# Optimization experiments

Hardware: AMD Instinct MI355X
Metric: run time of the kernel (lower is better)

Reference implementation:

```python
import math
import jax, jax.numpy as jnp
import numpy as np

B, N, TOKEN_DIM = 8, 8192, 512
NODE_DIM = 64
MAX_NODES = 64
SCORE_HIDDEN = 64


def setup_inputs() -> dict:
    key = jax.random.key(0)
    ks = jax.random.split(key, 8)
    s = lambda k, shape, fan_in: jax.random.normal(k, shape, jnp.float32) / np.sqrt(fan_in)
    return {
        "token_feats": jax.random.normal(ks[0], (B, N, TOKEN_DIM), jnp.float32),
        "score_w1": s(ks[1], (TOKEN_DIM, SCORE_HIDDEN), TOKEN_DIM),
        "score_b1": jnp.zeros((SCORE_HIDDEN,), jnp.float32),
        "score_w2": s(ks[2], (SCORE_HIDDEN, 1), SCORE_HIDDEN),
        "score_b2": jnp.zeros((1,), jnp.float32),
        "t2n_w": s(ks[3], (TOKEN_DIM, NODE_DIM), TOKEN_DIM),
        "n2t_w": s(ks[4], (NODE_DIM, TOKEN_DIM), NODE_DIM),
        "gcn_w1": s(ks[5], (NODE_DIM, NODE_DIM), NODE_DIM),
        "gcn_w2": s(ks[6], (NODE_DIM, NODE_DIM), NODE_DIM),
    }


def reference(token_feats, score_w1, score_b1, score_w2, score_b2,
              t2n_w, n2t_w, gcn_w1, gcn_w2):
    Bn, Nn, d = token_feats.shape
    M = MAX_NODES
    eps = 1e-6

    # --- node selection (scores -> threshold -> top-k among selected) ---
    h = jax.nn.relu(jnp.einsum('bnd,dh->bnh', token_feats, score_w1) + score_b1)
    scores = (jnp.einsum('bnh,ho->bno', h, score_w2) + score_b2)[..., 0]  # [B,N]
    mean = scores.mean(axis=1, keepdims=True)
    std = scores.std(axis=1, keepdims=True)  # unbiased=False (population)
    thr = mean + 0.5 * std
    count = jnp.sum(scores > thr, axis=1)  # [B]
    fallback_k = min(M, max(4, Nn // 16))
    take_k = jnp.where(count == 0, fallback_k, jnp.minimum(count, M))  # [B]

    _, top_idx = jax.lax.top_k(scores, M)  # [B,M] highest scores; set == torch's selection
    node_mask = jnp.arange(M)[None, :] < take_k[:, None]  # [B,M] bool
    maskf = node_mask.astype(token_feats.dtype)

    gathered = jnp.take_along_axis(token_feats, top_idx[..., None], axis=1)  # [B,M,d]
    H0 = jnp.einsum('bmd,dk->bmk', gathered, t2n_w) * maskf[..., None]  # [B,M,node_dim]

    # --- cosine-similarity adjacency, masked, self-loops, row-normalized ---
    nrm = jnp.maximum(jnp.linalg.norm(H0, axis=-1, keepdims=True), eps)
    Hn = H0 / nrm
    A = jax.nn.relu(jnp.einsum('bik,bjk->bij', Hn, Hn))
    A = A * (maskf[:, :, None] * maskf[:, None, :])
    A = A + jnp.eye(M, dtype=A.dtype)[None] * maskf[:, None, :]
    A = A / jnp.maximum(A.sum(axis=-1, keepdims=True), 1e-6)

    # --- two-layer GCN (no bias) ---
    x = jax.nn.relu(jnp.einsum('bij,bjk,kl->bil', A, H0, gcn_w1))
    Hg = jax.nn.relu(jnp.einsum('bij,bjk,kl->bil', A, x, gcn_w2))  # [B,M,node_dim]

    # --- attention scatter-back to tokens ---
    token_proj = jnp.einsum('bnd,dk->bnk', token_feats, t2n_w)  # [B,N,node_dim]
    logits = jnp.einsum('bnk,bmk->bnm', token_proj, Hg) / math.sqrt(NODE_DIM)
    attn = jax.nn.softmax(logits, axis=-1)
    injected = jnp.einsum('bnm,bmk->bnk', attn, Hg)
    back = jnp.einsum('bnk,kd->bnd', injected, n2t_w)
    return token_feats + back
```

## Files before the change

### kernel.cpp

```cpp
#include <hip/hip_runtime.h>
#include <hip/hip_bf16.h>

#define B_ 8
#define N_ 8192
#define D_ 512
#define M_ 64

typedef unsigned short u16;
typedef unsigned int u32;
typedef __attribute__((ext_vector_type(8))) short bf16x8;
typedef __attribute__((ext_vector_type(4))) float f32x4;

__device__ __forceinline__ u16 f2bf(float f) {
  u32 u = __float_as_uint(f);
  u += 0x7FFFu + ((u >> 16) & 1u);
  return (u16)(u >> 16);
}
__device__ __forceinline__ float bf2f(u16 h) {
  return __uint_as_float(((u32)h) << 16);
}

__device__ __forceinline__ int bfrag_idx(int kd, int c, int ncols16) {
  int sub = (kd >> 5) * ncols16 + (c >> 4);
  int lane = (c & 15) + 16 * ((kd & 15) >> 2);
  int e = (kd & 3) + 4 * ((kd >> 4) & 1);
  return sub * 512 + lane * 8 + e;
}

__device__ __forceinline__ int kslot(int ln, int e) {
  return (e & 3) + 4 * (ln >> 4) + 16 * (e >> 2);
}

__device__ __forceinline__ bf16x8 pack8(float4 v0, float4 v1) {
  bf16x8 a;
  a[0] = (short)f2bf(v0.x); a[1] = (short)f2bf(v0.y);
  a[2] = (short)f2bf(v0.z); a[3] = (short)f2bf(v0.w);
  a[4] = (short)f2bf(v1.x); a[5] = (short)f2bf(v1.y);
  a[6] = (short)f2bf(v1.z); a[7] = (short)f2bf(v1.w);
  return a;
}

__global__ __launch_bounds__(256) void k_prep(
    const float* __restrict__ t2n, const float* __restrict__ n2t,
    const float* __restrict__ W1, const float* __restrict__ g1,
    const float* __restrict__ g2,
    u16* __restrict__ t2nf, u16* __restrict__ n2tf,
    u16* __restrict__ W1h, u16* __restrict__ W1l,
    u16* __restrict__ g1f, u16* __restrict__ g2f)
{
  const int gid = blockIdx.x * 256 + threadIdx.x;
  const int stride = gridDim.x * 256;
  for (int s = gid; s < 512 * 64; s += stride) {
    const int k = s >> 6, c = s & 63;
    const int idx = bfrag_idx(k, c, 4);
    t2nf[idx] = f2bf(t2n[s]);
    const float w = W1[s];
    const u16 wh = f2bf(w);
    W1h[idx] = wh;
    W1l[idx] = f2bf(w - bf2f(wh));
  }
  for (int s = gid; s < 64 * 512; s += stride) {
    const int k = s >> 9, c = s & 511;
    n2tf[bfrag_idx(k, c, 32)] = f2bf(n2t[s]);
  }
  for (int s = gid; s < 4096; s += stride) {
    const int k = s >> 6, c = s & 63;
    g1f[bfrag_idx(k, c, 4)] = f2bf(g1[s]);
    g2f[bfrag_idx(k, c, 4)] = f2bf(g2[s]);
  }
}

__global__ __launch_bounds__(256, 4) void k_sp(
    const float* __restrict__ X, const u16* __restrict__ W1h,
    const u16* __restrict__ W1l, const u16* __restrict__ t2nf,
    const float* __restrict__ b1, const float* __restrict__ w2,
    const float* __restrict__ b2, float* __restrict__ scores,
    float* __restrict__ outStash)
{
  __shared__ __align__(16) u16 sB[2][6144];
  __shared__ __align__(16) u16 sAf[4096];
  const int tid = threadIdx.x;
  const int t0 = blockIdx.x * 64;
  const int wv = tid >> 6, ln = tid & 63;
  const int lq = ln >> 4, lr = ln & 15;
  u16* mySf = &sAf[wv * 1024];
  const float* xr = X + (size_t)(t0 + 16 * wv + lr) * D_;

  f32x4 acc[4], accP[4];
  #pragma unroll
  for (int cb = 0; cb < 4; ++cb) {
    acc[cb] = (f32x4){0.f, 0.f, 0.f, 0.f};
    accP[cb] = (f32x4){0.f, 0.f, 0.f, 0.f};
  }

  auto gsrc = [&](int f, int kb) -> const u16* {
    const int cb = f / 3, mat = f % 3;
    const u16* mp = (mat == 0) ? W1h : (mat == 1) ? W1l : t2nf;
    return mp + (kb * 4 + cb) * 512 + ln * 8;
  };

  bf16x8 wr[3];
  #pragma unroll
  for (int j = 0; j < 3; ++j)
    *(bf16x8*)&sB[0][(j * 4 + wv) * 512 + ln * 8] = *(const bf16x8*)gsrc(j * 4 + wv, 0);
  #pragma unroll
  for (int j = 0; j < 3; ++j) wr[j] = *(const bf16x8*)gsrc(j * 4 + wv, 1);
  float4 va0 = *(const float4*)(xr + 4 * lq);
  float4 va1 = *(const float4*)(xr + 16 + 4 * lq);
  __syncthreads();

  for (int kb = 0; kb < 16; ++kb) {
    const int cur = kb & 1;
    if (kb < 15) {
      #pragma unroll
      for (int j = 0; j < 3; ++j)
        *(bf16x8*)&sB[cur ^ 1][(j * 4 + wv) * 512 + ln * 8] = wr[j];
    }
    if (kb < 14) {
      #pragma unroll
      for (int j = 0; j < 3; ++j) wr[j] = *(const bf16x8*)gsrc(j * 4 + wv, kb + 2);
    }
    const float4 v0 = va0, v1 = va1;
    if (kb < 15) {
      va0 = *(const float4*)(xr + 32 * (kb + 1) + 4 * lq);
      va1 = *(const float4*)(xr + 32 * (kb + 1) + 16 + 4 * lq);
    }
    const float xs[8] = {v0.x, v0.y, v0.z, v0.w, v1.x, v1.y, v1.z, v1.w};
    bf16x8 ah, al;
    #pragma unroll
    for (int e = 0; e < 8; ++e) {
      const u16 h = f2bf(xs[e]);
      ah[e] = (short)h;
      al[e] = (short)f2bf(xs[e] - bf2f(h));
    }
    #pragma unroll
    for (int cb = 0; cb < 4; ++cb) {
      const bf16x8 bh = *(const bf16x8*)&sB[cur][(cb * 3 + 0) * 512 + ln * 8];
      const bf16x8 bl = *(const bf16x8*)&sB[cur][(cb * 3 + 1) * 512 + ln * 8];
      const bf16x8 bt = *(const bf16x8*)&sB[cur][(cb * 3 + 2) * 512 + ln * 8];
      acc[cb]  = __builtin_amdgcn_mfma_f32_16x16x32_bf16(ah, bh, acc[cb], 0, 0, 0);
      acc[cb]  = __builtin_amdgcn_mfma_f32_16x16x32_bf16(ah, bl, acc[cb], 0, 0, 0);
      acc[cb]  = __builtin_amdgcn_mfma_f32_16x16x32_bf16(al, bh, acc[cb], 0, 0, 0);
      accP[cb] = __builtin_amdgcn_mfma_f32_16x16x32_bf16(ah, bt, accP[cb], 0, 0, 0);
    }
    __syncthreads();
  }

  float b1v[4], w2v[4];
  #pragma unroll
  for (int cb = 0; cb < 4; ++cb) {
    const int col = cb * 16 + lr;
    b1v[cb] = b1[col]; w2v[cb] = w2[col];
  }
  const float b2v = b2[0];
  #pragma unroll
  for (int r = 0; r < 4; ++r) {
    float p = 0.f;
    #pragma unroll
    for (int cb = 0; cb < 4; ++cb) {
      const float h = fmaxf(acc[cb][r] + b1v[cb], 0.f);
      p = fmaf(h, w2v[cb], p);
    }
    p += __shfl_xor(p, 1); p += __shfl_xor(p, 2);
    p += __shfl_xor(p, 4); p += __shfl_xor(p, 8);
    if (lr == 0) scores[t0 + wv * 16 + 4 * lq + r] = p + b2v;
  }

  #pragma unroll
  for (int cb = 0; cb < 4; ++cb)
    #pragma unroll
    for (int r = 0; r < 4; ++r) {
      const int idx = (cb >> 1) * 512 + (4 * lq + r + 16 * (lr >> 2)) * 8 +
                      (lr & 3) + 4 * (cb & 1);
      mySf[idx] = f2bf(accP[cb][r]);
    }
  u16* stash = (u16*)(outStash + (size_t)blockIdx.x * 32768);
  #pragma unroll
  for (int kb2 = 0; kb2 < 2; ++kb2)
    *(bf16x8*)&stash[wv * 1024 + kb2 * 512 + ln * 8] =
        *(const bf16x8*)&mySf[kb2 * 512 + ln * 8];
}

__global__ __launch_bounds__(1024) void k_select(
    const float* __restrict__ scores, int* __restrict__ top_idx,
    int* __restrict__ take_k)
{
  __shared__ u32 hist[2048];
  __shared__ float redf[34];
  __shared__ u32 redu[16];
  __shared__ u32 scanp[16];
  __shared__ int sPivotBin;
  __shared__ u32 sTake, sNA, sCntA, sCntT;
  __shared__ int candIdx[64];
  __shared__ u32 candKey[64];
  __shared__ int tieIdx[1024];
  __shared__ u32 tieKey[1024];
  const int b = blockIdx.x, tid = threadIdx.x;
  const int wv = tid >> 6, ln = tid & 63;
  const float* s = scores + (size_t)b * N_;

  hist[tid] = 0; hist[tid + 1024] = 0;
  if (tid == 0) { sCntA = 0; sCntT = 0; }

  float v[8]; u32 key[8];
  float sum = 0.f, sq = 0.f;
  #pragma unroll
  for (int j = 0; j < 8; ++j) {
    v[j] = s[tid + j * 1024];
    sum += v[j]; sq = fmaf(v[j], v[j], sq);
    const u32 u = __float_as_uint(v[j]);
    key[j] = u ^ ((u32)((int)u >> 31) | 0x80000000u);
  }
  #pragma unroll
  for (int off = 32; off > 0; off >>= 1) {
    sum += __shfl_xor(sum, off);
    sq  += __shfl_xor(sq, off);
  }
  if (ln == 0) { redf[wv] = sum; redf[16 + wv] = sq; }
  __syncthreads();

  #pragma unroll
  for (int j = 0; j < 8; ++j) atomicAdd(&hist[key[j] >> 21], 1u);
  if (tid < 16) {
    float a = redf[tid], q = redf[16 + tid];
    #pragma unroll
    for (int off = 8; off > 0; off >>= 1) {
      a += __shfl_down(a, off);
      q += __shfl_down(q, off);
    }
    if (tid == 0) {
      const float mean = a / (float)N_;
      const float var = q / (float)N_ - mean * mean;
      redf[32] = mean + 0.5f * sqrtf(fmaxf(var, 0.f));
    }
  }
  __syncthreads();
  const float thr = redf[32];

  int c = 0;
  #pragma unroll
  for (int j = 0; j < 8; ++j) c += (v[j] > thr) ? 1 : 0;
  #pragma unroll
  for (int off = 32; off > 0; off >>= 1) c += __shfl_xor(c, off);
  if (ln == 0) redu[wv] = (u32)c;

  const u32 h_hi = hist[2 * tid], h_lo = hist[2 * tid + 1];
  const u32 ps = h_hi + h_lo;
  u32 run = ps;
  #pragma unroll
  for (int off = 1; off < 64; off <<= 1) {
    const u32 t = (u32)__shfl((int)run, ln + off);
    if (ln + off < 64) run += t;
  }
  if (ln == 0) scanp[wv] = run;
  __syncthreads();

  if (tid < 16) {
    u32 a = redu[tid];
    #pragma unroll
    for (int off = 8; off > 0; off >>= 1) a += (u32)__shfl_down((int)a, off);
    if (tid == 0) {
      const int cnt = (int)a;
      take_k[b] = (cnt == 0) ? M_ : (cnt < M_ ? cnt : M_);
    }
  }
  {
    u32 ws = 0;
    for (int w = wv + 1; w < 16; ++w) ws += scanp[w];
    const u32 suffIncl = run + ws;
    const u32 cumMid = suffIncl - h_hi;
    const u32 cumNext = suffIncl - ps;
    if (suffIncl >= 64u && cumMid < 64u) {
      sPivotBin = 2 * tid; sTake = 64u - cumMid; sNA = cumMid;
    }
    if (cumMid >= 64u && cumNext < 64u) {
      sPivotBin = 2 * tid + 1; sTake = 64u - cumNext; sNA = cumNext;
    }
  }
  __syncthreads();

  const int pb = sPivotBin;
  #pragma unroll
  for (int j = 0; j < 8; ++j) {
    const int bin = (int)(key[j] >> 21);
    if (bin > pb) {
      const u32 p = atomicAdd(&sCntA, 1u);
      candIdx[p] = tid + j * 1024; candKey[p] = key[j];
    } else if (bin == pb) {
      const u32 p = atomicAdd(&sCntT, 1u);
      if (p < 1024u) { tieIdx[p] = tid + j * 1024; tieKey[p] = key[j]; }
    }
  }
  __syncthreads();

  const int nA = (int)sNA;
  const int need = (int)sTake;
  const int T = (int)(sCntT < 1024u ? sCntT : 1024u);
  for (int t = tid; t < T; t += 1024) {
    const u32 k0 = tieKey[t]; const int i0 = tieIdx[t];
    int rk = 0;
    for (int q = 0; q < T; ++q) {
      const u32 kq = tieKey[q]; const int iq = tieIdx[q];
      rk += (kq > k0 || (kq == k0 && iq < i0)) ? 1 : 0;
    }
    if (rk < need) { candIdx[nA + rk] = i0; candKey[nA + rk] = k0; }
  }
  __syncthreads();

  if (tid < 64) {
    const u32 k0 = candKey[tid]; const int i0 = candIdx[tid];
    int rk = 0;
    for (int q = 0; q < 64; ++q) {
      const u32 kq = candKey[q]; const int iq = candIdx[q];
      rk += (kq > k0 || (kq == k0 && iq < i0)) ? 1 : 0;
    }
    top_idx[b * M_ + rk] = i0;
  }
}

__device__ __forceinline__ bf16x8 ldsA_frag(const float (*S)[65], int g, int kb, int ln) {
  const int lr = ln & 15;
  bf16x8 a;
  #pragma unroll
  for (int e = 0; e < 8; ++e) a[e] = (short)f2bf(S[16 * g + lr][32 * kb + kslot(ln, e)]);
  return a;
}
__device__ __forceinline__ bf16x8 ldsB_frag(const float (*S)[65], int cb, int kb, int ln) {
  const int lr = ln & 15;
  bf16x8 bb;
  #pragma unroll
  for (int e = 0; e < 8; ++e) bb[e] = (short)f2bf(S[32 * kb + kslot(ln, e)][16 * cb + lr]);
  return bb;
}
__device__ __forceinline__ bf16x8 ldsBT_frag(const float (*S)[65], int cb, int kb, int ln) {
  const int lr = ln & 15;
  bf16x8 bb;
  #pragma unroll
  for (int e = 0; e < 8; ++e) bb[e] = (short)f2bf(S[16 * cb + lr][32 * kb + kslot(ln, e)]);
  return bb;
}

__global__ __launch_bounds__(512) void k_graph(
    const float* __restrict__ X, const u16* __restrict__ t2nf,
    const u16* __restrict__ n2tf, const u16* __restrict__ g1f,
    const u16* __restrict__ g2f, const int* __restrict__ top_idx,
    const int* __restrict__ take_k, u16* __restrict__ HgTf,
    u16* __restrict__ Wf)
{
  __shared__ float sH0[64][65];
  __shared__ float sA[64][65];
  __shared__ float sT[64][65];
  __shared__ float sU[64][65];
  __shared__ float sR[64];
  const int b = blockIdx.x, tid = threadIdx.x;
  const int wv = tid >> 6, ln = tid & 63;
  const int lq = ln >> 4, lr = ln & 15;
  const int g = wv & 3;
  const int hh = wv >> 2;
  const int tk = take_k[b];
  const int rowm = 16 * g + 4 * lq;

  const int gidx = top_idx[b * M_ + 16 * g + lr];
  const float* xr = X + ((size_t)b * N_ + gidx) * D_;
  f32x4 d[2];
  #pragma unroll
  for (int cc = 0; cc < 2; ++cc) d[cc] = (f32x4){0.f, 0.f, 0.f, 0.f};
  {
    float4 p0[3], p1[3];
    #pragma unroll
    for (int q = 0; q < 3; ++q) {
      p0[q] = *(const float4*)(xr + 32 * q + 4 * lq);
      p1[q] = *(const float4*)(xr + 32 * q + 16 + 4 * lq);
    }
    #pragma unroll
    for (int kb = 0; kb < 16; ++kb) {
      const int slot = kb % 3;
      const float4 v0 = p0[slot], v1 = p1[slot];
      if (kb + 3 < 16) {
        p0[slot] = *(const float4*)(xr + 32 * (kb + 3) + 4 * lq);
        p1[slot] = *(const float4*)(xr + 32 * (kb + 3) + 16 + 4 * lq);
      }
      const bf16x8 a = pack8(v0, v1);
      #pragma unroll
      for (int cc = 0; cc < 2; ++cc) {
        const int cb = 2 * hh + cc;
        const bf16x8 bb = *(const bf16x8*)&t2nf[(kb * 4 + cb) * 512 + ln * 8];
        d[cc] = __builtin_amdgcn_mfma_f32_16x16x32_bf16(a, bb, d[cc], 0, 0, 0);
      }
    }
  }
  #pragma unroll
  for (int cc = 0; cc < 2; ++cc)
    #pragma unroll
    for (int r = 0; r < 4; ++r)
      sH0[rowm + r][16 * (2 * hh + cc) + lr] = (rowm + r < tk) ? d[cc][r] : 0.f;
  __syncthreads();

  if (tid < 64) {
    float ss = 0.f;
    #pragma unroll
    for (int k = 0; k < 64; ++k) { const float vv = sH0[tid][k]; ss = fmaf(vv, vv, ss); }
    sR[tid] = 1.f / fmaxf(sqrtf(ss), 1e-6f);
  }
  __syncthreads();
  #pragma unroll
  for (int p = 0; p < 8; ++p) {
    const int o = tid + p * 512;
    sU[o >> 6][o & 63] = sH0[o >> 6][o & 63] * sR[o >> 6];
  }
  __syncthreads();

  #pragma unroll
  for (int cc = 0; cc < 2; ++cc) d[cc] = (f32x4){0.f, 0.f, 0.f, 0.f};
  #pragma unroll
  for (int kb = 0; kb < 2; ++kb) {
    const bf16x8 a = ldsA_frag(sU, g, kb, ln);
    #pragma unroll
    for (int cc = 0; cc < 2; ++cc)
      d[cc] = __builtin_amdgcn_mfma_f32_16x16x32_bf16(a, ldsBT_frag(sU, 2 * hh + cc, kb, ln), d[cc], 0, 0, 0);
  }
  __syncthreads();
  #pragma unroll
  for (int cc = 0; cc < 2; ++cc)
    #pragma unroll
    for (int r = 0; r < 4; ++r) {
      const int row = rowm + r, col = 16 * (2 * hh + cc) + lr;
      float ss = fmaxf(d[cc][r], 0.f);
      ss = (row < tk && col < tk) ? ss : 0.f;
      if (row == col && row < tk) ss += 1.f;
      sA[row][col] = ss;
    }
  __syncthreads();

  if (tid < 64) {
    float rs = 0.f;
    #pragma unroll
    for (int j = 0; j < 64; ++j) rs += sA[tid][j];
    sR[tid] = 1.f / fmaxf(rs, 1e-6f);
  }
  __syncthreads();
  #pragma unroll
  for (int p = 0; p < 8; ++p) {
    const int o = tid + p * 512;
    sA[o >> 6][o & 63] *= sR[o >> 6];
  }
  __syncthreads();

  #pragma unroll
  for (int cc = 0; cc < 2; ++cc) d[cc] = (f32x4){0.f, 0.f, 0.f, 0.f};
  #pragma unroll
  for (int kb = 0; kb < 2; ++kb) {
    const bf16x8 a = ldsA_frag(sA, g, kb, ln);
    #pragma unroll
    for (int cc = 0; cc < 2; ++cc)
      d[cc] = __builtin_amdgcn_mfma_f32_16x16x32_bf16(a, ldsB_frag(sH0, 2 * hh + cc, kb, ln), d[cc], 0, 0, 0);
  }
  __syncthreads();
  #pragma unroll
  for (int cc = 0; cc < 2; ++cc)
    #pragma unroll
    for (int r = 0; r < 4; ++r) sT[rowm + r][16 * (2 * hh + cc) + lr] = d[cc][r];
  __syncthreads();

  #pragma unroll
  for (int cc = 0; cc < 2; ++cc) d[cc] = (f32x4){0.f, 0.f, 0.f, 0.f};
  #pragma unroll
  for (int kb = 0; kb < 2; ++kb) {
    const bf16x8 a = ldsA_frag(sT, g, kb, ln);
    #pragma unroll
    for (int cc = 0; cc < 2; ++cc) {
      const bf16x8 bb = *(const bf16x8*)&g1f[(kb * 4 + 2 * hh + cc) * 512 + ln * 8];
      d[cc] = __builtin_amdgcn_mfma_f32_16x16x32_bf16(a, bb, d[cc], 0, 0, 0);
    }
  }
  __syncthreads();
  #pragma unroll
  for (int cc = 0; cc < 2; ++cc)
    #pragma unroll
    for (int r = 0; r < 4; ++r)
      sU[rowm + r][16 * (2 * hh + cc) + lr] = fmaxf(d[cc][r], 0.f);
  __syncthreads();

  #pragma unroll
  for (int cc = 0; cc < 2; ++cc) d[cc] = (f32x4){0.f, 0.f, 0.f, 0.f};
  #pragma unroll
  for (int kb = 0; kb < 2; ++kb) {
    const bf16x8 a = ldsA_frag(sA, g, kb, ln);
    #pragma unroll
    for (int cc = 0; cc < 2; ++cc)
      d[cc] = __builtin_amdgcn_mfma_f32_16x16x32_bf16(a, ldsB_frag(sU, 2 * hh + cc, kb, ln), d[cc], 0, 0, 0);
  }
  __syncthreads();
  #pragma unroll
  for (int cc = 0; cc < 2; ++cc)
    #pragma unroll
    for (int r = 0; r < 4; ++r) sT[rowm + r][16 * (2 * hh + cc) + lr] = d[cc][r];
  __syncthreads();

  #pragma unroll
  for (int cc = 0; cc < 2; ++cc) d[cc] = (f32x4){0.f, 0.f, 0.f, 0.f};
  #pragma unroll
  for (int kb = 0; kb < 2; ++kb) {
    const bf16x8 a = ldsA_frag(sT, g, kb, ln);
    #pragma unroll
    for (int cc = 0; cc < 2; ++cc) {
      const bf16x8 bb = *(const bf16x8*)&g2f[(kb * 4 + 2 * hh + cc) * 512 + ln * 8];
      d[cc] = __builtin_amdgcn_mfma_f32_16x16x32_bf16(a, bb, d[cc], 0, 0, 0);
    }
  }
  __syncthreads();
  #pragma unroll
  for (int cc = 0; cc < 2; ++cc)
    #pragma unroll
    for (int r = 0; r < 4; ++r) {
      const int node = rowm + r, feat = 16 * (2 * hh + cc) + lr;
      const float hv = fmaxf(d[cc][r], 0.f);
      HgTf[(size_t)b * 4096 + bfrag_idx(feat, node, 4)] = f2bf(hv);
      sU[node][feat] = hv;
    }
  __syncthreads();

  for (int chkc = 0; chkc < 2; ++chkc) {
    const int chk = 2 * hh + chkc;
    f32x4 aw[8];
    #pragma unroll
    for (int c8 = 0; c8 < 8; ++c8) aw[c8] = (f32x4){0.f, 0.f, 0.f, 0.f};
    #pragma unroll
    for (int kbf = 0; kbf < 2; ++kbf) {
      const bf16x8 a = ldsA_frag(sU, g, kbf, ln);
      #pragma unroll
      for (int c8 = 0; c8 < 8; ++c8) {
        const bf16x8 bb = *(const bf16x8*)&n2tf[(kbf * 32 + chk * 8 + c8) * 512 + ln * 8];
        aw[c8] = __builtin_amdgcn_mfma_f32_16x16x32_bf16(a, bb, aw[c8], 0, 0, 0);
      }
    }
    #pragma unroll
    for (int c8 = 0; c8 < 8; ++c8)
      #pragma unroll
      for (int r = 0; r < 4; ++r) {
        const int m = 16 * g + 4 * lq + r;
        const int cc2 = (chk * 8 + c8) * 16 + lr;
        Wf[(size_t)b * 32768 + bfrag_idx(m, cc2, 32)] = f2bf(aw[c8][r]);
      }
  }
}

__global__ __launch_bounds__(256) void k_attn(
    const float* __restrict__ X, const u16* __restrict__ HgTf,
    const u16* __restrict__ Wf, float* __restrict__ out)
{
  __shared__ __align__(16) u16 sAf[4096];
  __shared__ __align__(16) float sBo[4][16][68];
  const int tid = threadIdx.x;
  const int b = blockIdx.x >> 7;
  const int t0 = (blockIdx.x & 127) << 6;
  const float* Xb = X + (size_t)b * N_ * D_;
  float* Ob = out + (size_t)b * N_ * D_;
  const int wv = tid >> 6, ln = tid & 63;
  const int lq = ln >> 4, lr = ln & 15;
  u16* mySf = &sAf[wv * 1024];
  const u16* stash = (const u16*)(out + (size_t)blockIdx.x * 32768);

  f32x4 accL[4];
  #pragma unroll
  for (int cb = 0; cb < 4; ++cb) accL[cb] = (f32x4){0.f, 0.f, 0.f, 0.f};
  #pragma unroll
  for (int kb = 0; kb < 2; ++kb) {
    const bf16x8 a = *(const bf16x8*)&stash[wv * 1024 + kb * 512 + ln * 8];
    #pragma unroll
    for (int cb = 0; cb < 4; ++cb) {
      const bf16x8 bb = *(const bf16x8*)&HgTf[(size_t)b * 4096 + (kb * 4 + cb) * 512 + ln * 8];
      accL[cb] = __builtin_amdgcn_mfma_f32_16x16x32_bf16(a, bb, accL[cb], 0, 0, 0);
    }
  }
  __syncthreads();

  float attnv[4][4];
  #pragma unroll
  for (int r = 0; r < 4; ++r) {
    const float v0 = accL[0][r], v1 = accL[1][r], v2 = accL[2][r], v3 = accL[3][r];
    float mx = fmaxf(fmaxf(v0, v1), fmaxf(v2, v3));
    mx = fmaxf(mx, __shfl_xor(mx, 1)); mx = fmaxf(mx, __shfl_xor(mx, 2));
    mx = fmaxf(mx, __shfl_xor(mx, 4)); mx = fmaxf(mx, __shfl_xor(mx, 8));
    const float e0 = __expf((v0 - mx) * 0.125f), e1 = __expf((v1 - mx) * 0.125f);
    const float e2 = __expf((v2 - mx) * 0.125f), e3 = __expf((v3 - mx) * 0.125f);
    float sm = (e0 + e1) + (e2 + e3);
    sm += __shfl_xor(sm, 1); sm += __shfl_xor(sm, 2);
    sm += __shfl_xor(sm, 4); sm += __shfl_xor(sm, 8);
    const float inv = 1.f / sm;
    attnv[0][r] = e0 * inv; attnv[1][r] = e1 * inv;
    attnv[2][r] = e2 * inv; attnv[3][r] = e3 * inv;
  }
  #pragma unroll
  for (int cb = 0; cb < 4; ++cb)
    #pragma unroll
    for (int r = 0; r < 4; ++r) {
      const int idx = (cb >> 1) * 512 + (4 * lq + r + 16 * (lr >> 2)) * 8 +
                      (lr & 3) + 4 * (cb & 1);
      mySf[idx] = f2bf(attnv[cb][r]);
    }

  for (int chk = 0; chk < 4; ++chk) {
    float4 xres[8];
    #pragma unroll
    for (int h = 0; h < 2; ++h)
      #pragma unroll
      for (int j = 0; j < 4; ++j)
        xres[h * 4 + j] = *(const float4*)(
            Xb + (size_t)(t0 + 16 * wv + 4 * j + lq) * D_ + chk * 128 + h * 64 + 4 * lr);

    f32x4 accB[8];
    #pragma unroll
    for (int c8 = 0; c8 < 8; ++c8) accB[c8] = (f32x4){0.f, 0.f, 0.f, 0.f};
    #pragma unroll
    for (int kb = 0; kb < 2; ++kb) {
      const bf16x8 a = *(const bf16x8*)&mySf[kb * 512 + ln * 8];
      #pragma unroll
      for (int c8 = 0; c8 < 8; ++c8) {
        const bf16x8 bb = *(const bf16x8*)&Wf[(size_t)b * 32768 + (kb * 32 + chk * 8 + c8) * 512 + ln * 8];
        accB[c8] = __builtin_amdgcn_mfma_f32_16x16x32_bf16(a, bb, accB[c8], 0, 0, 0);
      }
    }
    #pragma unroll
    for (int h = 0; h < 2; ++h) {
      #pragma unroll
      for (int c4 = 0; c4 < 4; ++c4)
        #pragma unroll
        for (int r = 0; r < 4; ++r)
          sBo[wv][4 * lq + r][c4 * 16 + lr] = accB[4 * h + c4][r];
      #pragma unroll
      for (int j = 0; j < 4; ++j) {
        const int rloc = 4 * j + lq;
        float4 vv = *(const float4*)&sBo[wv][rloc][4 * lr];
        const float4 xv = xres[h * 4 + j];
        vv.x += xv.x; vv.y += xv.y; vv.z += xv.z; vv.w += xv.w;
        *(float4*)(Ob + (size_t)(t0 + 16 * wv + rloc) * D_ + chk * 128 + h * 64 + 4 * lr) = vv;
      }
    }
  }
}

extern "C" void kernel_launch(void* const* d_in, const int* in_sizes, int n_in,
                              void* d_out, int out_size, void* d_ws, size_t ws_size,
                              hipStream_t stream)
{
  (void)in_sizes; (void)n_in; (void)out_size; (void)ws_size;
  const float* X   = (const float*)d_in[0];
  const float* W1  = (const float*)d_in[1];
  const float* b1  = (const float*)d_in[2];
  const float* w2  = (const float*)d_in[3];
  const float* b2  = (const float*)d_in[4];
  const float* t2n = (const float*)d_in[5];
  const float* n2t = (const float*)d_in[6];
  const float* g1  = (const float*)d_in[7];
  const float* g2  = (const float*)d_in[8];
  float* out = (float*)d_out;

  char* ws = (char*)d_ws;
  float* scores = (float*)(ws);
  u16* t2nf     = (u16*)(ws + 262144);
  u16* n2tf     = (u16*)(ws + 327680);
  u16* W1h      = (u16*)(ws + 393216);
  u16* W1l      = (u16*)(ws + 458752);
  u16* HgTf     = (u16*)(ws + 524288);
  u16* g1f      = (u16*)(ws + 589824);
  u16* g2f      = (u16*)(ws + 598016);
  int* top_idx  = (int*)(ws + 606208);
  int* take_k   = (int*)(ws + 608256);
  u16* Wf       = (u16*)(ws + 609280);

  k_prep<<<64, 256, 0, stream>>>(t2n, n2t, W1, g1, g2, t2nf, n2tf, W1h, W1l, g1f, g2f);
  k_sp<<<1024, 256, 0, stream>>>(X, W1h, W1l, t2nf, b1, w2, b2, scores, out);
  k_select<<<B_, 1024, 0, stream>>>(scores, top_idx, take_k);
  k_graph<<<B_, 512, 0, stream>>>(X, t2nf, n2tf, g1f, g2f, top_idx, take_k, HgTf, Wf);
  k_attn<<<1024, 256, 0, stream>>>(X, HgTf, Wf, out);
}
```

Measured before the change: 123.4 us.

## Fuse top-k selection and graph kernels into one 1024-thread block per batch

Merges the selection kernel and the graph/GCN kernel into a single kernel with one block per batch. Top indices and take_k now stay in shared memory instead of going through global memory, which removes one launch and the global round trip. The graph stage is remapped from 512 threads handling two column blocks each to 1024 threads handling one each. Shared memory per block grows because the selection and graph buffers now coexist.

```diff
diff --git a/kernel.cpp b/kernel.cpp
--- a/kernel.cpp
+++ b/kernel.cpp
@@ -181,9 +181,33 @@
         *(const bf16x8*)&mySf[kb2 * 512 + ln * 8];
 }
 
-__global__ __launch_bounds__(1024) void k_select(
-    const float* __restrict__ scores, int* __restrict__ top_idx,
-    int* __restrict__ take_k)
+__device__ __forceinline__ bf16x8 ldsA_frag(const float (*S)[65], int g, int kb, int ln) {
+  const int lr = ln & 15;
+  bf16x8 a;
+  #pragma unroll
+  for (int e = 0; e < 8; ++e) a[e] = (short)f2bf(S[16 * g + lr][32 * kb + kslot(ln, e)]);
+  return a;
+}
+__device__ __forceinline__ bf16x8 ldsB_frag(const float (*S)[65], int cb, int kb, int ln) {
+  const int lr = ln & 15;
+  bf16x8 bb;
+  #pragma unroll
+  for (int e = 0; e < 8; ++e) bb[e] = (short)f2bf(S[32 * kb + kslot(ln, e)][16 * cb + lr]);
+  return bb;
+}
+__device__ __forceinline__ bf16x8 ldsBT_frag(const float (*S)[65], int cb, int kb, int ln) {
+  const int lr = ln & 15;
+  bf16x8 bb;
+  #pragma unroll
+  for (int e = 0; e < 8; ++e) bb[e] = (short)f2bf(S[16 * cb + lr][32 * kb + kslot(ln, e)]);
+  return bb;
+}
+
+__global__ __launch_bounds__(1024) void k_selgraph(
+    const float* __restrict__ scores, const float* __restrict__ X,
+    const u16* __restrict__ t2nf, const u16* __restrict__ n2tf,
+    const u16* __restrict__ g1f, const u16* __restrict__ g2f,
+    u16* __restrict__ HgTf, u16* __restrict__ Wf)
 {
   __shared__ u32 hist[2048];
   __shared__ float redf[34];
@@ -195,8 +219,17 @@
   __shared__ u32 candKey[64];
   __shared__ int tieIdx[1024];
   __shared__ u32 tieKey[1024];
+  __shared__ int sTop[64];
+  __shared__ int sTkS;
+  __shared__ float sH0[64][65];
+  __shared__ float sA[64][65];
+  __shared__ float sT[64][65];
+  __shared__ float sU[64][65];
+  __shared__ float sR[64];
+
   const int b = blockIdx.x, tid = threadIdx.x;
   const int wv = tid >> 6, ln = tid & 63;
+  const int lq = ln >> 4, lr = ln & 15;
   const float* s = scores + (size_t)b * N_;
 
   hist[tid] = 0; hist[tid + 1024] = 0;
@@ -261,7 +294,7 @@
     for (int off = 8; off > 0; off >>= 1) a += (u32)__shfl_down((int)a, off);
     if (tid == 0) {
       const int cnt = (int)a;
-      take_k[b] = (cnt == 0) ? M_ : (cnt < M_ ? cnt : M_);
+      sTkS = (cnt == 0) ? M_ : (cnt < M_ ? cnt : M_);
     }
   }
   {
@@ -314,58 +347,20 @@
       const u32 kq = candKey[q]; const int iq = candIdx[q];
       rk += (kq > k0 || (kq == k0 && iq < i0)) ? 1 : 0;
     }
-    top_idx[b * M_ + rk] = i0;
-  }
-}
-
-__device__ __forceinline__ bf16x8 ldsA_frag(const float (*S)[65], int g, int kb, int ln) {
-  const int lr = ln & 15;
-  bf16x8 a;
-  #pragma unroll
-  for (int e = 0; e < 8; ++e) a[e] = (short)f2bf(S[16 * g + lr][32 * kb + kslot(ln, e)]);
-  return a;
-}
-__device__ __forceinline__ bf16x8 ldsB_frag(const float (*S)[65], int cb, int kb, int ln) {
-  const int lr = ln & 15;
-  bf16x8 bb;
-  #pragma unroll
-  for (int e = 0; e < 8; ++e) bb[e] = (short)f2bf(S[32 * kb + kslot(ln, e)][16 * cb + lr]);
-  return bb;
-}
-__device__ __forceinline__ bf16x8 ldsBT_frag(const float (*S)[65], int cb, int kb, int ln) {
-  const int lr = ln & 15;
-  bf16x8 bb;
-  #pragma unroll
-  for (int e = 0; e < 8; ++e) bb[e] = (short)f2bf(S[16 * cb + lr][32 * kb + kslot(ln, e)]);
-  return bb;
-}
-
-__global__ __launch_bounds__(512) void k_graph(
-    const float* __restrict__ X, const u16* __restrict__ t2nf,
-    const u16* __restrict__ n2tf, const u16* __restrict__ g1f,
-    const u16* __restrict__ g2f, const int* __restrict__ top_idx,
-    const int* __restrict__ take_k, u16* __restrict__ HgTf,
-    u16* __restrict__ Wf)
-{
-  __shared__ float sH0[64][65];
-  __shared__ float sA[64][65];
-  __shared__ float sT[64][65];
-  __shared__ float sU[64][65];
-  __shared__ float sR[64];
-  const int b = blockIdx.x, tid = threadIdx.x;
-  const int wv = tid >> 6, ln = tid & 63;
-  const int lq = ln >> 4, lr = ln & 15;
+    sTop[rk] = i0;
+  }
+  __syncthreads();
+
   const int g = wv & 3;
-  const int hh = wv >> 2;
-  const int tk = take_k[b];
+  const int cq = wv >> 2;
+  const int tk = sTkS;
   const int rowm = 16 * g + 4 * lq;
-
-  const int gidx = top_idx[b * M_ + 16 * g + lr];
-  const float* xr = X + ((size_t)b * N_ + gidx) * D_;
-  f32x4 d[2];
-  #pragma unroll
-  for (int cc = 0; cc < 2; ++cc) d[cc] = (f32x4){0.f, 0.f, 0.f, 0.f};
+  f32x4 d;
+
   {
+    const int gidx = sTop[16 * g + lr];
+    const float* xr = X + ((size_t)b * N_ + gidx) * D_;
+    d = (f32x4){0.f, 0.f, 0.f, 0.f};
     float4 p0[3], p1[3];
     #pragma unroll
     for (int q = 0; q < 3; ++q) {
@@ -381,19 +376,13 @@
         p1[slot] = *(const float4*)(xr + 32 * (kb + 3) + 16 + 4 * lq);
       }
       const bf16x8 a = pack8(v0, v1);
-      #pragma unroll
-      for (int cc = 0; cc < 2; ++cc) {
-        const int cb = 2 * hh + cc;
-        const bf16x8 bb = *(const bf16x8*)&t2nf[(kb * 4 + cb) * 512 + ln * 8];
-        d[cc] = __builtin_amdgcn_mfma_f32_16x16x32_bf16(a, bb, d[cc], 0, 0, 0);
-      }
-    }
-  }
-  #pragma unroll
-  for (int cc = 0; cc < 2; ++cc)
+      const bf16x8 bb = *(const bf16x8*)&t2nf[(kb * 4 + cq) * 512 + ln * 8];
+      d = __builtin_amdgcn_mfma_f32_16x16x32_bf16(a, bb, d, 0, 0, 0);
+    }
     #pragma unroll
     for (int r = 0; r < 4; ++r)
-      sH0[rowm + r][16 * (2 * hh + cc) + lr] = (rowm + r < tk) ? d[cc][r] : 0.f;
+      sH0[rowm + r][16 * cq + lr] = (rowm + r < tk) ? d[r] : 0.f;
+  }
   __syncthreads();
 
   if (tid < 64) {
@@ -404,32 +393,26 @@
   }
   __syncthreads();
   #pragma unroll
-  for (int p = 0; p < 8; ++p) {
-    const int o = tid + p * 512;
+  for (int p = 0; p < 4; ++p) {
+    const int o = tid + p * 1024;
     sU[o >> 6][o & 63] = sH0[o >> 6][o & 63] * sR[o >> 6];
   }
   __syncthreads();
 
-  #pragma unroll
-  for (int cc = 0; cc < 2; ++cc) d[cc] = (f32x4){0.f, 0.f, 0.f, 0.f};
-  #pragma unroll
-  for (int kb = 0; kb < 2; ++kb) {
-    const bf16x8 a = ldsA_frag(sU, g, kb, ln);
-    #pragma unroll
-    for (int cc = 0; cc < 2; ++cc)
-      d[cc] = __builtin_amdgcn_mfma_f32_16x16x32_bf16(a, ldsBT_frag(sU, 2 * hh + cc, kb, ln), d[cc], 0, 0, 0);
-  }
-  __syncthreads();
-  #pragma unroll
-  for (int cc = 0; cc < 2; ++cc)
-    #pragma unroll
-    for (int r = 0; r < 4; ++r) {
-      const int row = rowm + r, col = 16 * (2 * hh + cc) + lr;
-      float ss = fmaxf(d[cc][r], 0.f);
-      ss = (row < tk && col < tk) ? ss : 0.f;
-      if (row == col && row < tk) ss += 1.f;
-      sA[row][col] = ss;
-    }
+  d = (f32x4){0.f, 0.f, 0.f, 0.f};
+  #pragma unroll
+  for (int kb = 0; kb < 2; ++kb)
+    d = __builtin_amdgcn_mfma_f32_16x16x32_bf16(ldsA_frag(sU, g, kb, ln),
+                                                ldsBT_frag(sU, cq, kb, ln), d, 0, 0, 0);
+  __syncthreads();
+  #pragma unroll
+  for (int r = 0; r < 4; ++r) {
+    const int row = rowm + r, col = 16 * cq + lr;
+    float ss = fmaxf(d[r], 0.f);
+    ss = (row < tk && col < tk) ? ss : 0.f;
+    if (row == col && row < tk) ss += 1.f;
+    sA[row][col] = ss;
+  }
   __syncthreads();
 
   if (tid < 64) {
@@ -440,88 +423,61 @@
   }
   __syncthreads();
   #pragma unroll
-  for (int p = 0; p < 8; ++p) {
-    const int o = tid + p * 512;
+  for (int p = 0; p < 4; ++p) {
+    const int o = tid + p * 1024;
     sA[o >> 6][o & 63] *= sR[o >> 6];
   }
   __syncthreads();
 
-  #pragma unroll
-  for (int cc = 0; cc < 2; ++cc) d[cc] = (f32x4){0.f, 0.f, 0.f, 0.f};
+  d = (f32x4){0.f, 0.f, 0.f, 0.f};
+  #pragma unroll
+  for (int kb = 0; kb < 2; ++kb)
+    d = __builtin_amdgcn_mfma_f32_16x16x32_bf16(ldsA_frag(sA, g, kb, ln),
+                                                ldsB_frag(sH0, cq, kb, ln), d, 0, 0, 0);
+  __syncthreads();
+  #pragma unroll
+  for (int r = 0; r < 4; ++r) sT[rowm + r][16 * cq + lr] = d[r];
+  __syncthreads();
+
+  d = (f32x4){0.f, 0.f, 0.f, 0.f};
   #pragma unroll
   for (int kb = 0; kb < 2; ++kb) {
-    const bf16x8 a = ldsA_frag(sA, g, kb, ln);
-    #pragma unroll
-    for (int cc = 0; cc < 2; ++cc)
-      d[cc] = __builtin_amdgcn_mfma_f32_16x16x32_bf16(a, ldsB_frag(sH0, 2 * hh + cc, kb, ln), d[cc], 0, 0, 0);
-  }
-  __syncthreads();
-  #pragma unroll
-  for (int cc = 0; cc < 2; ++cc)
-    #pragma unroll
-    for (int r = 0; r < 4; ++r) sT[rowm + r][16 * (2 * hh + cc) + lr] = d[cc][r];
-  __syncthreads();
-
-  #pragma unroll
-  for (int cc = 0; cc < 2; ++cc) d[cc] = (f32x4){0.f, 0.f, 0.f, 0.f};
+    const bf16x8 bb = *(const bf16x8*)&g1f[(kb * 4 + cq) * 512 + ln * 8];
+    d = __builtin_amdgcn_mfma_f32_16x16x32_bf16(ldsA_frag(sT, g, kb, ln), bb, d, 0, 0, 0);
+  }
+  __syncthreads();
+  #pragma unroll
+  for (int r = 0; r < 4; ++r) sU[rowm + r][16 * cq + lr] = fmaxf(d[r], 0.f);
+  __syncthreads();
+
+  d = (f32x4){0.f, 0.f, 0.f, 0.f};
+  #pragma unroll
+  for (int kb = 0; kb < 2; ++kb)
+    d = __builtin_amdgcn_mfma_f32_16x16x32_bf16(ldsA_frag(sA, g, kb, ln),
+                                                ldsB_frag(sU, cq, kb, ln), d, 0, 0, 0);
+  __syncthreads();
+  #pragma unroll
+  for (int r = 0; r < 4; ++r) sT[rowm + r][16 * cq + lr] = d[r];
+  __syncthreads();
+
+  d = (f32x4){0.f, 0.f, 0.f, 0.f};
   #pragma unroll
   for (int kb = 0; kb < 2; ++kb) {
-    const bf16x8 a = ldsA_frag(sT, g, kb, ln);
-    #pragma unroll
-    for (int cc = 0; cc < 2; ++cc) {
-      const bf16x8 bb = *(const bf16x8*)&g1f[(kb * 4 + 2 * hh + cc) * 512 + ln * 8];
-      d[cc] = __builtin_amdgcn_mfma_f32_16x16x32_bf16(a, bb, d[cc], 0, 0, 0);
-    }
-  }
-  __syncthreads();
-  #pragma unroll
-  for (int cc = 0; cc < 2; ++cc)
-    #pragma unroll
-    for (int r = 0; r < 4; ++r)
-      sU[rowm + r][16 * (2 * hh + cc) + lr] = fmaxf(d[cc][r], 0.f);
-  __syncthreads();
-
-  #pragma unroll
-  for (int cc = 0; cc < 2; ++cc) d[cc] = (f32x4){0.f, 0.f, 0.f, 0.f};
-  #pragma unroll
-  for (int kb = 0; kb < 2; ++kb) {
-    const bf16x8 a = ldsA_frag(sA, g, kb, ln);
-    #pragma unroll
-    for (int cc = 0; cc < 2; ++cc)
-      d[cc] = __builtin_amdgcn_mfma_f32_16x16x32_bf16(a, ldsB_frag(sU, 2 * hh + cc, kb, ln), d[cc], 0, 0, 0);
-  }
-  __syncthreads();
-  #pragma unroll
-  for (int cc = 0; cc < 2; ++cc)
-    #pragma unroll
-    for (int r = 0; r < 4; ++r) sT[rowm + r][16 * (2 * hh + cc) + lr] = d[cc][r];
-  __syncthreads();
-
-  #pragma unroll
-  for (int cc = 0; cc < 2; ++cc) d[cc] = (f32x4){0.f, 0.f, 0.f, 0.f};
-  #pragma unroll
-  for (int kb = 0; kb < 2; ++kb) {
-    const bf16x8 a = ldsA_frag(sT, g, kb, ln);
-    #pragma unroll
-    for (int cc = 0; cc < 2; ++cc) {
-      const bf16x8 bb = *(const bf16x8*)&g2f[(kb * 4 + 2 * hh + cc) * 512 + ln * 8];
-      d[cc] = __builtin_amdgcn_mfma_f32_16x16x32_bf16(a, bb, d[cc], 0, 0, 0);
-    }
-  }
-  __syncthreads();
-  #pragma unroll
-  for (int cc = 0; cc < 2; ++cc)
-    #pragma unroll
-    for (int r = 0; r < 4; ++r) {
-      const int node = rowm + r, feat = 16 * (2 * hh + cc) + lr;
-      const float hv = fmaxf(d[cc][r], 0.f);
-      HgTf[(size_t)b * 4096 + bfrag_idx(feat, node, 4)] = f2bf(hv);
-      sU[node][feat] = hv;
-    }
-  __syncthreads();
-
-  for (int chkc = 0; chkc < 2; ++chkc) {
-    const int chk = 2 * hh + chkc;
+    const bf16x8 bb = *(const bf16x8*)&g2f[(kb * 4 + cq) * 512 + ln * 8];
+    d = __builtin_amdgcn_mfma_f32_16x16x32_bf16(ldsA_frag(sT, g, kb, ln), bb, d, 0, 0, 0);
+  }
+  __syncthreads();
+  #pragma unroll
+  for (int r = 0; r < 4; ++r) {
+    const int node = rowm + r, feat = 16 * cq + lr;
+    const float hv = fmaxf(d[r], 0.f);
+    HgTf[(size_t)b * 4096 + bfrag_idx(feat, node, 4)] = f2bf(hv);
+    sU[node][feat] = hv;
+  }
+  __syncthreads();
+
+  {
+    const int chk = cq;
     f32x4 aw[8];
     #pragma unroll
     for (int c8 = 0; c8 < 8; ++c8) aw[c8] = (f32x4){0.f, 0.f, 0.f, 0.f};
@@ -665,13 +621,10 @@
   u16* HgTf     = (u16*)(ws + 524288);
   u16* g1f      = (u16*)(ws + 589824);
   u16* g2f      = (u16*)(ws + 598016);
-  int* top_idx  = (int*)(ws + 606208);
-  int* take_k   = (int*)(ws + 608256);
   u16* Wf       = (u16*)(ws + 609280);
 
   k_prep<<<64, 256, 0, stream>>>(t2n, n2t, W1, g1, g2, t2nf, n2tf, W1h, W1l, g1f, g2f);
   k_sp<<<1024, 256, 0, stream>>>(X, W1h, W1l, t2nf, b1, w2, b2, scores, out);
-  k_select<<<B_, 1024, 0, stream>>>(scores, top_idx, take_k);
-  k_graph<<<B_, 512, 0, stream>>>(X, t2nf, n2tf, g1f, g2f, top_idx, take_k, HgTf, Wf);
+  k_selgraph<<<B_, 1024, 0, stream>>>(scores, X, t2nf, n2tf, g1f, g2f, HgTf, Wf);
   k_attn<<<1024, 256, 0, stream>>>(X, HgTf, Wf, out);
 }
```

Measured after the change: 130.9 us. +6.1%, slower.
